# Optimization experiments

Measured on AMD Instinct MI355X. Metric: run time of the kernel, lower is better.

The kernel has to match this reference:

```python
import jax, jax.numpy as jnp
import numpy as np

SNAPPING_GAIN = 30.0


def setup_inputs() -> dict:
    key = jax.random.key(0)
    k1, k2 = jax.random.split(key)
    latent_coeffs = jax.random.normal(k1, (16, 2048, 1024), dtype=jnp.float32)
    # NMF basis is non-negative; 1024 atoms of dim 900 (30x30 ARC grids)
    basis_vectors = jax.random.uniform(k2, (1024, 900), dtype=jnp.float32)
    return {"latent_coeffs": latent_coeffs, "basis_vectors": basis_vectors}


def reference(latent_coeffs, basis_vectors):
    # [B, K, C] -> sharpened softmax over codes
    probs = jax.nn.softmax(latent_coeffs * SNAPPING_GAIN, axis=-1)
    indices = jnp.argmax(probs, axis=-1)                        # [B, K] int
    one_hot = jax.nn.one_hot(indices, probs.shape[-1], dtype=probs.dtype)
    # straight-through: value == one_hot, gradient flows through probs
    one_hot_st = probs + jax.lax.stop_gradient(one_hot - probs)
    # [B,K,C] @ [C,D] -> [B,K,D] (effectively a row-gather of the basis)
    quantized = jnp.einsum('bkc,cd->bkd', one_hot_st, basis_vectors)
    return quantized, indices
```

## Files before the change

kernel.cpp:

```cpp
#include <hip/hip_runtime.h>


#define C_DIM 1024
#define D_DIM 900
#define ROWS_PER_WAVE 2

typedef float vfloat4 __attribute__((ext_vector_type(4)));

__device__ __forceinline__ int wave_argmax(vfloat4 v0, vfloat4 v1, vfloat4 v2,
                                           vfloat4 v3, int lane) {
    float m = v0[0];
    int   mi = lane * 4;
    #pragma unroll
    for (int e = 1; e < 4; ++e)
        if (v0[e] > m) { m = v0[e]; mi = lane * 4 + e; }
    #pragma unroll
    for (int e = 0; e < 4; ++e)
        if (v1[e] > m) { m = v1[e]; mi = (64 + lane) * 4 + e; }
    #pragma unroll
    for (int e = 0; e < 4; ++e)
        if (v2[e] > m) { m = v2[e]; mi = (128 + lane) * 4 + e; }
    #pragma unroll
    for (int e = 0; e < 4; ++e)
        if (v3[e] > m) { m = v3[e]; mi = (192 + lane) * 4 + e; }

    #pragma unroll
    for (int off = 32; off > 0; off >>= 1) {
        float om = __shfl_xor(m, off, 64);
        int   oi = __shfl_xor(mi, off, 64);
        if (om > m || (om == m && oi < mi)) { m = om; mi = oi; }
    }
    return mi;
}

__device__ __forceinline__ void gather_store(const float* __restrict__ basis,
                                             float* __restrict__ out_q,
                                             int idx, size_t row, int lane) {
    const vfloat4* b4 = reinterpret_cast<const vfloat4*>(basis + (size_t)idx * D_DIM);
    vfloat4*       o4 = reinterpret_cast<vfloat4*>(out_q + row * D_DIM);
    #pragma unroll
    for (int j = 0; j < 4; ++j) {
        int t = 64 * j + lane;
        if (t < 225) {
            vfloat4 bv = b4[t];
            __builtin_nontemporal_store(bv, &o4[t]);
        }
    }
}

__global__ __launch_bounds__(256) void basisvq_kernel(
    const float* __restrict__ latent,
    const float* __restrict__ basis,
    float* __restrict__ out_q,
    float* __restrict__ out_idx,
    int rows)
{
    const int lane = threadIdx.x & 63;
    const int wv   = blockIdx.x * 4 + (threadIdx.x >> 6);
    const int r0   = wv * ROWS_PER_WAVE;
    if (r0 >= rows) return;

    const vfloat4* l0 = reinterpret_cast<const vfloat4*>(latent + (size_t)r0 * C_DIM);
    vfloat4 a0 = __builtin_nontemporal_load(&l0[lane]);
    vfloat4 a1 = __builtin_nontemporal_load(&l0[lane + 64]);
    vfloat4 a2 = __builtin_nontemporal_load(&l0[lane + 128]);
    vfloat4 a3 = __builtin_nontemporal_load(&l0[lane + 192]);

    const vfloat4* l1 = reinterpret_cast<const vfloat4*>(latent + (size_t)(r0 + 1) * C_DIM);
    vfloat4 b0 = __builtin_nontemporal_load(&l1[lane]);
    vfloat4 b1 = __builtin_nontemporal_load(&l1[lane + 64]);
    vfloat4 b2 = __builtin_nontemporal_load(&l1[lane + 128]);
    vfloat4 b3 = __builtin_nontemporal_load(&l1[lane + 192]);

    int idx0 = wave_argmax(a0, a1, a2, a3, lane);
    if (lane == 0) __builtin_nontemporal_store((float)idx0, &out_idx[r0]);
    gather_store(basis, out_q, idx0, (size_t)r0, lane);

    int idx1 = wave_argmax(b0, b1, b2, b3, lane);
    if (lane == 0) __builtin_nontemporal_store((float)idx1, &out_idx[r0 + 1]);
    gather_store(basis, out_q, idx1, (size_t)(r0 + 1), lane);
}

extern "C" void kernel_launch(void* const* d_in, const int* in_sizes, int n_in,
                              void* d_out, int out_size, void* d_ws, size_t ws_size,
                              hipStream_t stream) {
    const float* latent = (const float*)d_in[0];
    const float* basis  = (const float*)d_in[1];
    (void)n_in; (void)d_ws; (void)ws_size; (void)out_size;

    const int rows = in_sizes[0] / C_DIM;
    float* out_q   = (float*)d_out;
    float* out_idx = (float*)d_out + (size_t)rows * D_DIM;

    const int blocks = (rows + 8 - 1) / 8;
    basisvq_kernel<<<blocks, 256, 0, stream>>>(latent, basis, out_q, out_idx, rows);
}
```

Before: 54.21 us.

## Use persistent grid-stride waves with software-prefetched next row

Replaces the one-shot grid, where each wave handles two rows, with a fixed 2048-block persistent grid. Each wave strides over rows and prefetches the next row's latent data while it computes the argmax and gathers the basis row for the current one. The aim is to overlap latent loads with the gather/store traffic and cut wave launch overhead. In exchange each wave holds fewer loads in flight at once, and the fixed grid size may not match the CU count.

After: 54.21 us. About the same (+0.0%).

```diff
diff --git a/kernel.cpp b/kernel.cpp
--- a/kernel.cpp
+++ b/kernel.cpp
@@ -3,7 +3,6 @@
 
 #define C_DIM 1024
 #define D_DIM 900
-#define ROWS_PER_WAVE 2
 
 typedef float vfloat4 __attribute__((ext_vector_type(4)));
 
@@ -33,21 +32,6 @@
     return mi;
 }
 
-__device__ __forceinline__ void gather_store(const float* __restrict__ basis,
-                                             float* __restrict__ out_q,
-                                             int idx, size_t row, int lane) {
-    const vfloat4* b4 = reinterpret_cast<const vfloat4*>(basis + (size_t)idx * D_DIM);
-    vfloat4*       o4 = reinterpret_cast<vfloat4*>(out_q + row * D_DIM);
-    #pragma unroll
-    for (int j = 0; j < 4; ++j) {
-        int t = 64 * j + lane;
-        if (t < 225) {
-            vfloat4 bv = b4[t];
-            __builtin_nontemporal_store(bv, &o4[t]);
-        }
-    }
-}
-
 __global__ __launch_bounds__(256) void basisvq_kernel(
     const float* __restrict__ latent,
     const float* __restrict__ basis,
@@ -57,28 +41,47 @@
 {
     const int lane = threadIdx.x & 63;
     const int wv   = blockIdx.x * 4 + (threadIdx.x >> 6);
-    const int r0   = wv * ROWS_PER_WAVE;
-    if (r0 >= rows) return;
+    const int NW   = gridDim.x * 4;
 
-    const vfloat4* l0 = reinterpret_cast<const vfloat4*>(latent + (size_t)r0 * C_DIM);
-    vfloat4 a0 = __builtin_nontemporal_load(&l0[lane]);
-    vfloat4 a1 = __builtin_nontemporal_load(&l0[lane + 64]);
-    vfloat4 a2 = __builtin_nontemporal_load(&l0[lane + 128]);
-    vfloat4 a3 = __builtin_nontemporal_load(&l0[lane + 192]);
+    int row = wv;
+    vfloat4 c0, c1, c2, c3;
+    if (row < rows) {
+        const vfloat4* lr = reinterpret_cast<const vfloat4*>(latent + (size_t)row * C_DIM);
+        c0 = __builtin_nontemporal_load(&lr[lane]);
+        c1 = __builtin_nontemporal_load(&lr[lane + 64]);
+        c2 = __builtin_nontemporal_load(&lr[lane + 128]);
+        c3 = __builtin_nontemporal_load(&lr[lane + 192]);
+    }
 
-    const vfloat4* l1 = reinterpret_cast<const vfloat4*>(latent + (size_t)(r0 + 1) * C_DIM);
-    vfloat4 b0 = __builtin_nontemporal_load(&l1[lane]);
-    vfloat4 b1 = __builtin_nontemporal_load(&l1[lane + 64]);
-    vfloat4 b2 = __builtin_nontemporal_load(&l1[lane + 128]);
-    vfloat4 b3 = __builtin_nontemporal_load(&l1[lane + 192]);
+    while (row < rows) {
+        const int nrow = row + NW;
 
-    int idx0 = wave_argmax(a0, a1, a2, a3, lane);
-    if (lane == 0) __builtin_nontemporal_store((float)idx0, &out_idx[r0]);
-    gather_store(basis, out_q, idx0, (size_t)r0, lane);
+        vfloat4 n0, n1, n2, n3;
+        if (nrow < rows) {
+            const vfloat4* ln = reinterpret_cast<const vfloat4*>(latent + (size_t)nrow * C_DIM);
+            n0 = __builtin_nontemporal_load(&ln[lane]);
+            n1 = __builtin_nontemporal_load(&ln[lane + 64]);
+            n2 = __builtin_nontemporal_load(&ln[lane + 128]);
+            n3 = __builtin_nontemporal_load(&ln[lane + 192]);
+        }
 
-    int idx1 = wave_argmax(b0, b1, b2, b3, lane);
-    if (lane == 0) __builtin_nontemporal_store((float)idx1, &out_idx[r0 + 1]);
-    gather_store(basis, out_q, idx1, (size_t)(r0 + 1), lane);
+        const int idx = wave_argmax(c0, c1, c2, c3, lane);
+        if (lane == 0) out_idx[row] = (float)idx;
+
+        const vfloat4* b4 = reinterpret_cast<const vfloat4*>(basis + (size_t)idx * D_DIM);
+        vfloat4*       o4 = reinterpret_cast<vfloat4*>(out_q + (size_t)row * D_DIM);
+        #pragma unroll
+        for (int j = 0; j < 4; ++j) {
+            int t = 64 * j + lane;
+            if (t < 225) {
+                vfloat4 bv = b4[t];
+                __builtin_nontemporal_store(bv, &o4[t]);
+            }
+        }
+
+        row = nrow;
+        c0 = n0; c1 = n1; c2 = n2; c3 = n3;
+    }
 }
 
 extern "C" void kernel_launch(void* const* d_in, const int* in_sizes, int n_in,
@@ -92,6 +95,6 @@
     float* out_q   = (float*)d_out;
     float* out_idx = (float*)d_out + (size_t)rows * D_DIM;
 
-    const int blocks = (rows + 8 - 1) / 8;
+    const int blocks = 2048;
     basisvq_kernel<<<blocks, 256, 0, stream>>>(latent, basis, out_q, out_idx, rows);
 }
```
